# Optimization experiments

Hardware: AMD Instinct MI355X
Metric: run time of the kernel (lower is better)

Reference implementation:

```python
import jax, jax.numpy as jnp
import numpy as np

TAU = 2.0      # LIF membrane time constant
VTH = 1.0      # spike threshold
ALPHA = 2.0    # surrogate-gradient sharpness (atan surrogate)
EPS = 1e-5     # BatchNorm eps

@jax.custom_vjp
def spike(u):
    return (u > 0.0).astype(u.dtype)

def _spike_fwd(u):
    return spike(u), u

def _spike_bwd(u, g):
    sg = ALPHA / (2.0 * (1.0 + (jnp.pi / 2.0 * ALPHA * u) ** 2))
    return (g * sg,)

spike.defvjp(_spike_fwd, _spike_bwd)

def lif_time(x):
    # x: [B,T,C,H,W] -> spikes [B,T,C,H,W]; hard-reset LIF, v0 = 0
    xT = jnp.moveaxis(x, 1, 0)  # [T,B,C,H,W]
    def step(v, xt):
        v = v + (xt - v) / TAU
        s = spike(v - VTH)
        return v * (1.0 - s), s
    _, sT = jax.lax.scan(step, jnp.zeros_like(xT[0]), xT)
    return jnp.moveaxis(sT, 0, 1)

def conv2d(x, w, stride, pad):
    return jax.lax.conv_general_dilated(
        x, w, (stride, stride), [(pad, pad), (pad, pad)],
        dimension_numbers=('NCHW', 'OIHW', 'NCHW'))

def bn(x, gamma, beta, mean, var):
    # inference-style BatchNorm2d with running stats; x: [N,C,H,W]
    inv = gamma * jax.lax.rsqrt(var + EPS)
    return x * inv[None, :, None, None] + (beta - mean * inv)[None, :, None, None]

def setup_inputs() -> dict:
    key = jax.random.key(0)
    ks = jax.random.split(key, 16)
    B, T, Cin, Cout, H, W = 16, 8, 128, 256, 56, 56
    d = {}
    d['x_spike'] = (jax.random.uniform(ks[0], (B, T, Cin, H, W)) < 0.2).astype(jnp.float32)
    d['conv1_w'] = jax.random.normal(ks[1], (Cout, Cin, 3, 3), dtype=jnp.float32) * 0.05
    d['conv2_w'] = jax.random.normal(ks[2], (Cout, Cout, 3, 3), dtype=jnp.float32) * 0.05
    d['ds_w'] = jax.random.normal(ks[3], (Cout, Cin, 1, 1), dtype=jnp.float32) * 0.05
    for i, p in enumerate(['n1', 'n2', 'nd']):
        d[p + '_gamma'] = 1.0 + 0.1 * jax.random.normal(ks[4 + i], (Cout,), dtype=jnp.float32)
        d[p + '_beta'] = 0.1 * jax.random.normal(ks[7 + i], (Cout,), dtype=jnp.float32)
        d[p + '_mean'] = 0.01 * jax.random.normal(ks[10 + i], (Cout,), dtype=jnp.float32)
        d[p + '_var'] = jax.random.uniform(ks[13 + i], (Cout,), minval=0.5, maxval=1.5)
    return d

def reference(x_spike, conv1_w, conv2_w, ds_w,
              n1_gamma, n1_beta, n1_mean, n1_var,
              n2_gamma, n2_beta, n2_mean, n2_var,
              nd_gamma, nd_beta, nd_mean, nd_var):
    B, T, Cin, H, W = x_spike.shape
    x_flat = x_spike.reshape(B * T, Cin, H, W)
    # downsample shortcut (1x1 conv stride 2 + BN)
    identity = bn(conv2d(x_flat, ds_w, 2, 0), nd_gamma, nd_beta, nd_mean, nd_var)
    # NOTE: original module runs lif_shortcut on identity but DISCARDS the result
    # (pure state side-effect); it does not affect the output, so it is omitted.
    out = bn(conv2d(x_flat, conv1_w, 2, 1), n1_gamma, n1_beta, n1_mean, n1_var)
    Cout, Ho, Wo = out.shape[1], out.shape[2], out.shape[3]
    out = lif_time(out.reshape(B, T, Cout, Ho, Wo))
    out = bn(conv2d(out.reshape(B * T, Cout, Ho, Wo), conv2_w, 1, 1),
             n2_gamma, n2_beta, n2_mean, n2_var) + identity
    return lif_time(out.reshape(B, T, Cout, Ho, Wo))
```

## Files before the change

kernel.cpp:

```cpp
#include <hip/hip_runtime.h>
#include <hip/hip_bf16.h>

#define CIN  128
#define CO   256
#define HIN  56
#define WIN  56
#define OH   28
#define OWW  28
#define P    784
#define HWIN 3136
#define PERT 200704

typedef __attribute__((ext_vector_type(4))) float f32x4;
typedef __attribute__((ext_vector_type(4))) int   i32x4;

__device__ __forceinline__ i32x4 mfma_i8_64(i32x4 a, i32x4 b, i32x4 c) {
    return __builtin_amdgcn_mfma_i32_16x16x64_i8(a, b, c, 0, 0, 0);
}

__device__ __forceinline__ void gld_lds16(const void* g, void* l) {
    __builtin_amdgcn_global_load_lds(
        (const __attribute__((address_space(1))) void*)g,
        (__attribute__((address_space(3))) void*)l, 16, 0, 0);
}

__global__ __launch_bounds__(256) void k_prep_bias(
    const float* __restrict__ g1, const float* __restrict__ b1,
    const float* __restrict__ m1, const float* __restrict__ v1,
    const float* __restrict__ g2, const float* __restrict__ b2,
    const float* __restrict__ m2, const float* __restrict__ v2,
    const float* __restrict__ gd, const float* __restrict__ bd,
    const float* __restrict__ md, const float* __restrict__ vd,
    float* __restrict__ inv1o, float* __restrict__ bias1o,
    float* __restrict__ inv2o, float* __restrict__ invdo,
    float* __restrict__ bias2o)
{
    int co = threadIdx.x;
    float inv1 = g1[co] / sqrtf(v1[co] + 1e-5f);
    float inv2 = g2[co] / sqrtf(v2[co] + 1e-5f);
    float invd = gd[co] / sqrtf(vd[co] + 1e-5f);
    inv1o[co]  = inv1;
    bias1o[co] = fmaf(-m1[co], inv1, b1[co]);
    inv2o[co]  = inv2;
    invdo[co]  = invd;
    bias2o[co] = fmaf(-m2[co], inv2, b2[co]) + fmaf(-md[co], invd, bd[co]);
}

__global__ __launch_bounds__(256) void k_prep_w1s(
    const float* __restrict__ w1, const float* __restrict__ inv1,
    float* __restrict__ qscale, float* __restrict__ scale1)
{
    int wv = (blockIdx.x * 256 + threadIdx.x) >> 6;
    int lane = threadIdx.x & 63;
    int co = wv;
    float iv = inv1[co];
    float m = 0.f;
    for (int k = lane; k < 1152; k += 64)
        m = fmaxf(m, fabsf(w1[(size_t)co * 1152 + k] * iv));
#pragma unroll
    for (int off = 32; off > 0; off >>= 1)
        m = fmaxf(m, __shfl_xor(m, off));
    if (lane == 0) {
        int s = (int)floorf(log2f(8355000.0f / m));
        if (s > 44) s = 44;
        qscale[co] = ldexpf(1.0f, s);
        scale1[co] = ldexpf(1.0f, -s);
    }
}

__global__ __launch_bounds__(256) void k_prep_w1i8(
    const float* __restrict__ w1, const float* __restrict__ inv1,
    const float* __restrict__ qscale,
    signed char* __restrict__ pa, signed char* __restrict__ pb,
    signed char* __restrict__ pc)
{
    int i = blockIdx.x * 256 + threadIdx.x;
    if (i >= 18432) return;
    int tap = i >> 11;
    int r   = i & 2047;
    int kg  = r >> 10;
    int r2  = r & 1023;
    int lane = r2 & 63;
    int cf  = r2 >> 6;
    int co  = cf * 16 + (lane & 15);
    int ci0 = kg * 64 + (lane >> 4) * 16;
    float iv = inv1[co], q = qscale[co];
#pragma unroll
    for (int j = 0; j < 16; j++) {
        float w = w1[((size_t)co * CIN + ci0 + j) * 9 + tap] * iv;
        int W = __float2int_rn(w * q);
        int d0 = ((W & 0xFF) ^ 0x80) - 0x80;  W = (W - d0) / 256;
        int d1 = ((W & 0xFF) ^ 0x80) - 0x80;  W = (W - d1) / 256;
        size_t idx = (size_t)i * 16 + j;
        pa[idx] = (signed char)W;
        pb[idx] = (signed char)d1;
        pc[idx] = (signed char)d0;
    }
}

__global__ __launch_bounds__(256) void k_prep_w2s(
    const float* __restrict__ w2, const float* __restrict__ inv2,
    const float* __restrict__ wd, const float* __restrict__ invd,
    float* __restrict__ qscale, float* __restrict__ scale2)
{
    int wv = (blockIdx.x * 256 + threadIdx.x) >> 6;
    int lane = threadIdx.x & 63;
    int co = wv;
    float iv2 = inv2[co], ivd = invd[co];
    float m = 0.f;
    for (int k = lane; k < 2304; k += 64)
        m = fmaxf(m, fabsf(w2[(size_t)co * 2304 + k] * iv2));
    for (int k = lane; k < 128; k += 64)
        m = fmaxf(m, fabsf(wd[(size_t)co * 128 + k] * ivd));
#pragma unroll
    for (int off = 32; off > 0; off >>= 1)
        m = fmaxf(m, __shfl_xor(m, off));
    if (lane == 0) {
        int s = (int)floorf(log2f(8355000.0f / m));
        if (s > 40) s = 40;
        qscale[co] = ldexpf(1.0f, s);
        scale2[co] = ldexpf(1.0f, -s);
    }
}

__global__ __launch_bounds__(256) void k_prep_w2i8(
    const float* __restrict__ w2, const float* __restrict__ inv2,
    const float* __restrict__ qscale,
    signed char* __restrict__ pa, signed char* __restrict__ pb,
    signed char* __restrict__ pc)
{
    int i = blockIdx.x * 256 + threadIdx.x;
    if (i >= 36864) return;
    int tap = i >> 12;
    int r   = i & 4095;
    int kg  = r >> 10;
    int r2  = r & 1023;
    int cf  = r2 >> 6;
    int lane = r2 & 63;
    int co  = cf * 16 + (lane & 15);
    int ci0 = kg * 64 + (lane >> 4) * 16;
    float iv = inv2[co], q = qscale[co];
#pragma unroll
    for (int j = 0; j < 16; j++) {
        float w = w2[((size_t)co * CO + ci0 + j) * 9 + tap] * iv;
        int W = __float2int_rn(w * q);
        int d0 = ((W & 0xFF) ^ 0x80) - 0x80;  W = (W - d0) / 256;
        int d1 = ((W & 0xFF) ^ 0x80) - 0x80;  W = (W - d1) / 256;
        size_t idx = (size_t)i * 16 + j;
        pa[idx] = (signed char)W;
        pb[idx] = (signed char)d1;
        pc[idx] = (signed char)d0;
    }
}

__global__ __launch_bounds__(256) void k_prep_wdi8(
    const float* __restrict__ wd, const float* __restrict__ invd,
    const float* __restrict__ qscale,
    signed char* __restrict__ pa, signed char* __restrict__ pb,
    signed char* __restrict__ pc)
{
    int i = blockIdx.x * 256 + threadIdx.x;
    if (i >= 2048) return;
    int kg  = i >> 10;
    int r2  = i & 1023;
    int cf  = r2 >> 6;
    int lane = r2 & 63;
    int co  = cf * 16 + (lane & 15);
    int ci0 = kg * 64 + (lane >> 4) * 16;
    float iv = invd[co], q = qscale[co];
#pragma unroll
    for (int j = 0; j < 16; j++) {
        float w = wd[(size_t)co * CIN + ci0 + j] * iv;
        int W = __float2int_rn(w * q);
        int d0 = ((W & 0xFF) ^ 0x80) - 0x80;  W = (W - d0) / 256;
        int d1 = ((W & 0xFF) ^ 0x80) - 0x80;  W = (W - d1) / 256;
        size_t idx = (size_t)i * 16 + j;
        pa[idx] = (signed char)W;
        pb[idx] = (signed char)d1;
        pc[idx] = (signed char)d0;
    }
}

__global__ __launch_bounds__(256) void k_pack1(
    const float* __restrict__ x, unsigned int* __restrict__ xt_p)
{
    int i = blockIdx.x * 256 + threadIdx.x;
    int pos = i % HWIN;
    int nw  = i / HWIN;
    int w   = nw & 3;
    int n   = nw >> 2;
    const float* xp = x + ((size_t)n * CIN + w * 32) * HWIN + pos;
    unsigned int word = 0;
#pragma unroll
    for (int ci = 0; ci < 32; ci++)
        if (xp[(size_t)ci * HWIN] != 0.f) word |= (1u << ci);
    xt_p[((size_t)n * HWIN + pos) * 4 + w] = word;
}

__global__ __launch_bounds__(256) void k_conv1_mfma(
    const unsigned int* __restrict__ xt_p,
    const signed char* __restrict__ pa,
    const signed char* __restrict__ pb,
    const signed char* __restrict__ pc,
    const float* __restrict__ scale1,
    const float* __restrict__ bias1,
    float* __restrict__ out)
{
    __shared__ unsigned int XWP[2][522 * 2];

    const int n    = blockIdx.x / 7;
    const int rt   = blockIdx.x - n * 7;
    const int r0   = rt * 4;
    const int tid  = threadIdx.x;
    const int wave = tid >> 6;
    const int lane = tid & 63;
    const int l15  = lane & 15;
    const int quad = lane >> 4;
    const int cf   = blockIdx.y * 4 + wave;

    const unsigned int* xp_n = xt_p + (size_t)n * HWIN * 4;
    for (int i = tid; i < 513; i += 256) {
        int row = i / 57, c = i - row * 57;
        int irow = 2 * r0 - 1 + row;
        int iw   = c - 1;
        uint4 val = {0u, 0u, 0u, 0u};
        if (irow >= 0 && iw >= 0)
            val = *(const uint4*)(xp_n + (size_t)(irow * WIN + iw) * 4);
        int base = row * 58 + c;
        XWP[0][base * 2 + 0] = val.x;
        XWP[0][base * 2 + 1] = val.y;
        XWP[1][base * 2 + 0] = val.z;
        XWP[1][base * 2 + 1] = val.w;
    }
    __syncthreads();

    int ib[7];
#pragma unroll
    for (int f = 0; f < 7; f++) {
        int pos = f * 16 + l15;
        int rr = pos / 28, cc = pos - rr * 28;
        ib[f] = (2 * rr) * 58 + 2 * cc;
    }

    const int  qh = quad >> 1;
    const int  ql = (quad & 1) * 16;

    i32x4 accA[7], accB[7], accC[7];
#pragma unroll
    for (int f = 0; f < 7; f++) {
        accA[f] = (i32x4){0, 0, 0, 0};
        accB[f] = (i32x4){0, 0, 0, 0};
        accC[f] = (i32x4){0, 0, 0, 0};
    }

    i32x4 wa, wb, wc, na, nb, nc;
    {
        size_t b0 = (size_t)cf * 1024 + lane * 16;
        wa = *(const i32x4*)(pa + b0);
        wb = *(const i32x4*)(pb + b0);
        wc = *(const i32x4*)(pc + b0);
        na = wa; nb = wb; nc = wc;
    }

    for (int kg = 0; kg < 2; kg++) {
        for (int tap = 0; tap < 9; tap++) {
            int rd = kg * 9 + tap;
            if (rd < 17) {
                int rn = rd + 1, kn = rn / 9, tn = rn - kn * 9;
                size_t b0 = ((size_t)(tn * 2 + kn) * 16 + cf) * 1024 + lane * 16;
                na = *(const i32x4*)(pa + b0);
                nb = *(const i32x4*)(pb + b0);
                nc = *(const i32x4*)(pc + b0);
            }
            const int kh = tap / 3, kw = tap - kh * 3;
            const int tapoff = kh * 58 + kw;
#pragma unroll
            for (int f = 0; f < 7; f++) {
                int base = ib[f] + tapoff;
                uint2 pr = *(const uint2*)&XWP[kg][base * 2];
                unsigned int w32  = qh ? pr.y : pr.x;
                unsigned int bits = (w32 >> ql) & 0xFFFFu;
                uint4 u;
                u.x = ((bits & 15u)         * 0x00204081u) & 0x01010101u;
                u.y = (((bits >> 4) & 15u)  * 0x00204081u) & 0x01010101u;
                u.z = (((bits >> 8) & 15u)  * 0x00204081u) & 0x01010101u;
                u.w = ((bits >> 12)         * 0x00204081u) & 0x01010101u;
                union { uint4 q; i32x4 v; } cv;
                cv.q = u;
                accA[f] = mfma_i8_64(wa, cv.v, accA[f]);
                accB[f] = mfma_i8_64(wb, cv.v, accB[f]);
                accC[f] = mfma_i8_64(wc, cv.v, accC[f]);
            }
            wa = na; wb = nb; wc = nc;
        }
    }

#pragma unroll
    for (int f = 0; f < 7; f++) {
        int pg = rt * 112 + f * 16 + l15;
#pragma unroll
        for (int reg = 0; reg < 4; reg++) {
            int co = cf * 16 + quad * 4 + reg;
            float hi = (float)accA[f][reg];
            float mi = (float)accB[f][reg];
            float lo = (float)accC[f][reg];
            float val = fmaf(hi, 65536.f, fmaf(mi, 256.f, lo));
            out[((size_t)n * CO + co) * P + pg] = fmaf(val, scale1[co], bias1[co]);
        }
    }
}

__global__ __launch_bounds__(256) void k_lif1t(
    const float* __restrict__ pre, unsigned char* __restrict__ st)
{
    __shared__ unsigned short T[16 * 68];
    const int b   = blockIdx.x;
    const int co0 = blockIdx.y * 64;
    const int kg  = blockIdx.y;
    const int p0  = blockIdx.z * 16;
    const int tid  = threadIdx.x;
    const int pcol = tid & 15;
    const int g    = tid >> 4;
    const int pos = p0 + g;
    const int oh  = pos / 28, ow = pos - oh * 28;
    const int f8  = ((((oh + 1) * 30 + ow + 1) >> 1) & 3);
    const int no  = (pcol >> 2) ^ f8;
    const int wb  = (pcol & 3) * 4;
    float v[4] = {0.f, 0.f, 0.f, 0.f};
    for (int t = 0; t < 8; t++) {
        const float* src = pre + (((size_t)(b * 8 + t)) * CO + co0) * P + p0;
        unsigned short s[4];
#pragma unroll
        for (int j = 0; j < 4; j++) {
            int co = g + 16 * j;
            float xv = src[(size_t)co * P + pcol];
            v[j] = v[j] + (xv - v[j]) * 0.5f;
            bool sp = v[j] > 1.0f;
            s[j] = sp ? 1 : 0;
            if (sp) v[j] = 0.f;
        }
        __syncthreads();
#pragma unroll
        for (int j = 0; j < 4; j++) T[pcol * 68 + g + 16 * j] = s[j];
        __syncthreads();
        unsigned char* dst = st + (((size_t)(b * 8 + t) * 4 + kg) * P + pos) * 64
                               + no * 16 + wb;
        uchar4 ov;
        ov.x = (unsigned char)T[g * 68 + pcol * 4 + 0];
        ov.y = (unsigned char)T[g * 68 + pcol * 4 + 1];
        ov.z = (unsigned char)T[g * 68 + pcol * 4 + 2];
        ov.w = (unsigned char)T[g * 68 + pcol * 4 + 3];
        *(uchar4*)dst = ov;
    }
}

__global__ __launch_bounds__(256) void k_conv2_mfma(
    const unsigned char* __restrict__ spike_t,
    const unsigned int* __restrict__ xt_p,
    const signed char* __restrict__ p2a,
    const signed char* __restrict__ p2b,
    const signed char* __restrict__ p2c,
    const signed char* __restrict__ pda,
    const signed char* __restrict__ pdb,
    const signed char* __restrict__ pdc,
    const float* __restrict__ scale2,
    const float* __restrict__ bias2,
    float* __restrict__ out)
{
    __shared__ unsigned char SB[2 * 11520];
    __shared__ unsigned int  XW2[4 * 112];

    const int n    = blockIdx.x / 7;
    const int rt   = blockIdx.x - n * 7;
    const int r0   = rt * 4;
    const int tid  = threadIdx.x;
    const int wave = tid >> 6;
    const int lane = tid & 63;
    const int l15  = lane & 15;
    const int quad = lane >> 4;
    const int cf0  = blockIdx.y * 8 + wave * 2;

    {
        uint4 z = {0u, 0u, 0u, 0u};
        for (int i = tid; i < 1440; i += 256) ((uint4*)SB)[i] = z;
    }
    for (int i = tid; i < 112; i += 256) {
        int r = i / 28, c = i - r * 28;
        uint4 w4 = *(const uint4*)(xt_p + ((size_t)n * HWIN
                    + (2 * (r0 + r)) * WIN + 2 * c) * 4);
        XW2[0 * 112 + i] = w4.x;
        XW2[1 * 112 + i] = w4.y;
        XW2[2 * 112 + i] = w4.z;
        XW2[3 * 112 + i] = w4.w;
    }
    __syncthreads();

    int  g_irow[3], g_lds[3];
    bool g_ok[3];
    int  g_half[3];
#pragma unroll
    for (int k = 0; k < 3; k++) {
        int idx  = wave * 3 + k;
        int row  = idx >> 1, half = idx & 1;
        int irow = r0 - 1 + row;
        g_irow[k] = irow;
        g_half[k] = half;
        g_ok[k]   = ((unsigned)irow < 28u) && (half == 0 || lane < 48);
        g_lds[k]  = row * 1920 + 64 + half * 1024;
    }
    const char* sp_n = (const char*)spike_t + (size_t)n * 4 * P * 64;

#pragma unroll
    for (int k = 0; k < 3; k++)
        if (g_ok[k])
            gld_lds16(sp_n + (size_t)g_irow[k] * 1792 + g_half[k] * 1024 + lane * 16,
                      (char*)SB + g_lds[k]);

    int ib[7];
#pragma unroll
    for (int f = 0; f < 7; f++) {
        int pos = f * 16 + l15;
        int rr = pos / 28, cc = pos - rr * 28;
        ib[f] = rr * 30 + cc;
    }

    i32x4 acc[3][2][7];
#pragma unroll
    for (int p = 0; p < 3; p++)
#pragma unroll
        for (int g = 0; g < 2; g++)
#pragma unroll
            for (int f = 0; f < 7; f++) acc[p][g][f] = (i32x4){0, 0, 0, 0};

    for (int kg = 0; kg < 2; kg++) {
        size_t b0 = ((size_t)kg * 16 + cf0) * 1024 + (size_t)lane * 16;
        i32x4 d0[2], d1[2], d2[2];
#pragma unroll
        for (int g = 0; g < 2; g++) {
            d0[g] = *(const i32x4*)(pda + b0 + (size_t)g * 1024);
            d1[g] = *(const i32x4*)(pdb + b0 + (size_t)g * 1024);
            d2[g] = *(const i32x4*)(pdc + b0 + (size_t)g * 1024);
        }
        const int wsel = (kg * 2 + (quad >> 1)) * 112;
        const int shv  = (quad & 1) * 16;
#pragma unroll
        for (int f = 0; f < 7; f++) {
            unsigned int w32  = XW2[wsel + f * 16 + l15];
            unsigned int bits = (w32 >> shv) & 0xFFFFu;
            uint4 u;
            u.x = ((bits & 15u)         * 0x00204081u) & 0x01010101u;
            u.y = (((bits >> 4) & 15u)  * 0x00204081u) & 0x01010101u;
            u.z = (((bits >> 8) & 15u)  * 0x00204081u) & 0x01010101u;
            u.w = ((bits >> 12)         * 0x00204081u) & 0x01010101u;
            union { uint4 q; i32x4 v; } cv;
            cv.q = u;
#pragma unroll
            for (int g = 0; g < 2; g++) {
                acc[0][g][f] = mfma_i8_64(d0[g], cv.v, acc[0][g][f]);
                acc[1][g][f] = mfma_i8_64(d1[g], cv.v, acc[1][g][f]);
                acc[2][g][f] = mfma_i8_64(d2[g], cv.v, acc[2][g][f]);
            }
        }
    }
    __syncthreads();

    i32x4 cw[2][3], nx[2][3];
#pragma unroll
    for (int g = 0; g < 2; g++) {
        size_t b0 = ((size_t)(cf0 + g)) * 1024 + (size_t)lane * 16;
        cw[g][0] = *(const i32x4*)(p2a + b0);
        cw[g][1] = *(const i32x4*)(p2b + b0);
        cw[g][2] = *(const i32x4*)(p2c + b0);
        nx[g][0] = cw[g][0]; nx[g][1] = cw[g][1]; nx[g][2] = cw[g][2];
    }

    for (int c = 0; c < 4; c++) {
        if (c < 3) {
            const char* base = sp_n + (size_t)(c + 1) * 50176;
            char* dstb = (char*)SB + ((c + 1) & 1) * 11520;
#pragma unroll
            for (int k = 0; k < 3; k++)
                if (g_ok[k])
                    gld_lds16(base + (size_t)g_irow[k] * 1792 + g_half[k] * 1024 + lane * 16,
                              dstb + g_lds[k]);
        }
        const int bufsh = (c & 1) * 11520;
        for (int tap = 0; tap < 9; tap++) {
            int rd = c * 9 + tap;
            if (rd < 35) {
                int rn = rd + 1, cn = rn / 9, tn = rn - cn * 9;
                size_t b0 = ((size_t)(tn * 4 + cn) * 16 + cf0) * 1024
                          + (size_t)lane * 16;
#pragma unroll
                for (int g = 0; g < 2; g++) {
                    nx[g][0] = *(const i32x4*)(p2a + b0 + (size_t)g * 1024);
                    nx[g][1] = *(const i32x4*)(p2b + b0 + (size_t)g * 1024);
                    nx[g][2] = *(const i32x4*)(p2c + b0 + (size_t)g * 1024);
                }
            }
            const int kh = tap / 3, kw = tap - kh * 3;
            const int tapoff = kh * 30 + kw;
#pragma unroll
            for (int f = 0; f < 7; f++) {
                int slot = ib[f] + tapoff;
                int sw   = (slot >> 1) & 3;
                i32x4 bfr = *(const i32x4*)(
                    SB + bufsh + slot * 64 + ((quad ^ sw) * 16));
#pragma unroll
                for (int g = 0; g < 2; g++) {
                    acc[0][g][f] = mfma_i8_64(cw[g][0], bfr, acc[0][g][f]);
                    acc[1][g][f] = mfma_i8_64(cw[g][1], bfr, acc[1][g][f]);
                    acc[2][g][f] = mfma_i8_64(cw[g][2], bfr, acc[2][g][f]);
                }
            }
#pragma unroll
            for (int g = 0; g < 2; g++) {
                cw[g][0] = nx[g][0]; cw[g][1] = nx[g][1]; cw[g][2] = nx[g][2];
            }
        }
        __syncthreads();
    }

#pragma unroll
    for (int g = 0; g < 2; g++)
#pragma unroll
        for (int f = 0; f < 7; f++) {
            int pg = rt * 112 + f * 16 + l15;
#pragma unroll
            for (int reg = 0; reg < 4; reg++) {
                int co = (cf0 + g) * 16 + quad * 4 + reg;
                float A  = (float)acc[0][g][f][reg];
                float Bv = (float)acc[1][g][f][reg];
                float Cv = (float)acc[2][g][f][reg];
                float val = fmaf(A, 65536.f, fmaf(Bv, 256.f, Cv));
                out[((size_t)n * CO + co) * P + pg] = fmaf(val, scale2[co], bias2[co]);
            }
        }
}

__global__ __launch_bounds__(256) void k_lif4(const float4* __restrict__ in,
                                              float4* __restrict__ out)
{
    const int q = PERT / 4;
    const int i = blockIdx.x * 256 + threadIdx.x;
    const int b = i / q;
    const int r = i - b * q;
    const float4* pi = in  + (size_t)(b * 8) * q + r;
    float4*       po = out + (size_t)(b * 8) * q + r;
    float v0 = 0.f, v1 = 0.f, v2 = 0.f, v3 = 0.f;
#pragma unroll
    for (int t = 0; t < 8; t++) {
        float4 xt = pi[(size_t)t * q];
        float4 s;
        v0 = v0 + (xt.x - v0) * 0.5f; s.x = (v0 > 1.0f) ? 1.f : 0.f; if (v0 > 1.0f) v0 = 0.f;
        v1 = v1 + (xt.y - v1) * 0.5f; s.y = (v1 > 1.0f) ? 1.f : 0.f; if (v1 > 1.0f) v1 = 0.f;
        v2 = v2 + (xt.z - v2) * 0.5f; s.z = (v2 > 1.0f) ? 1.f : 0.f; if (v2 > 1.0f) v2 = 0.f;
        v3 = v3 + (xt.w - v3) * 0.5f; s.w = (v3 > 1.0f) ? 1.f : 0.f; if (v3 > 1.0f) v3 = 0.f;
        po[(size_t)t * q] = s;
    }
}

extern "C" void kernel_launch(void* const* d_in, const int* in_sizes, int n_in,
                              void* d_out, int out_size, void* d_ws, size_t ws_size,
                              hipStream_t stream) {
    const float* x   = (const float*)d_in[0];
    const float* w1  = (const float*)d_in[1];
    const float* w2  = (const float*)d_in[2];
    const float* wd  = (const float*)d_in[3];
    const float* n1g = (const float*)d_in[4];
    const float* n1b = (const float*)d_in[5];
    const float* n1m = (const float*)d_in[6];
    const float* n1v = (const float*)d_in[7];
    const float* n2g = (const float*)d_in[8];
    const float* n2b = (const float*)d_in[9];
    const float* n2m = (const float*)d_in[10];
    const float* n2v = (const float*)d_in[11];
    const float* ndg = (const float*)d_in[12];
    const float* ndb = (const float*)d_in[13];
    const float* ndm = (const float*)d_in[14];
    const float* ndv = (const float*)d_in[15];

    float* out = (float*)d_out;

    char* w = (char*)d_ws;
    unsigned char*  spike_t = (unsigned char*)w;
    signed char*    p2a     = (signed char*)(w + 25690112);
    signed char*    p2b     = (signed char*)(w + 26279936);
    signed char*    p2c     = (signed char*)(w + 26869760);
    signed char*    pa      = (signed char*)(w + 27459584);
    signed char*    pb      = (signed char*)(w + 27754496);
    signed char*    pc      = (signed char*)(w + 28049408);
    signed char*    pda     = (signed char*)(w + 28344320);
    signed char*    pdb     = (signed char*)(w + 28377088);
    signed char*    pdc     = (signed char*)(w + 28409856);
    float*          qscale1 = (float*)(w + 28442624);
    float*          scale1f = (float*)(w + 28443648);
    float*          qscale2 = (float*)(w + 28444672);
    float*          scale2f = (float*)(w + 28445696);
    float*          bias2   = (float*)(w + 28446720);
    float*          bias1   = (float*)(w + 28447744);
    float*          inv1    = (float*)(w + 28448768);
    float*          inv2    = (float*)(w + 28449792);
    float*          invd    = (float*)(w + 28450816);
    unsigned int*   xt_p    = (unsigned int*)(w + 28451840);

    k_prep_bias<<<1, 256, 0, stream>>>(n1g, n1b, n1m, n1v,
                                       n2g, n2b, n2m, n2v,
                                       ndg, ndb, ndm, ndv,
                                       inv1, bias1, inv2, invd, bias2);
    k_prep_w1s<<<64, 256, 0, stream>>>(w1, inv1, qscale1, scale1f);
    k_prep_w1i8<<<72, 256, 0, stream>>>(w1, inv1, qscale1, pa, pb, pc);
    k_prep_w2s<<<64, 256, 0, stream>>>(w2, inv2, wd, invd, qscale2, scale2f);
    k_prep_w2i8<<<144, 256, 0, stream>>>(w2, inv2, qscale2, p2a, p2b, p2c);
    k_prep_wdi8<<<8, 256, 0, stream>>>(wd, invd, qscale2, pda, pdb, pdc);

    k_pack1<<<(128 * 4 * HWIN) / 256, 256, 0, stream>>>(x, xt_p);
    k_conv1_mfma<<<dim3(896, 4), 256, 0, stream>>>(
        xt_p, pa, pb, pc, scale1f, bias1, out);
    k_lif1t<<<dim3(16, 4, 49), 256, 0, stream>>>(out, spike_t);
    k_conv2_mfma<<<dim3(896, 2), 256, 0, stream>>>(
        spike_t, xt_p, p2a, p2b, p2c, pda, pdb, pdc, scale2f, bias2, out);
    k_lif4<<<(16 * (PERT / 4)) / 256, 256, 0, stream>>>(
        (const float4*)out, (float4*)out);
}
```

Baseline: 726.1 us.

## Merge prep kernels, stage all conv2 channel groups in LDS, add MFMA priority

Seven small weight-prep and packing kernels are merged into two launches, with the BN inverse recomputed inline instead of stored, which cuts launch overhead. Conv2 now loads all four input-channel groups into a quadrupled LDS buffer up front and runs one flat 36-step loop with no per-chunk barriers. Downsample weights are hoisted into registers before the loop. s_setprio is raised around MFMA groups in both convs. The larger LDS footprint (about 46KB) may lower occupancy, and the extra registers for hoisted weights may raise register pressure.

```diff
diff --git a/kernel.cpp b/kernel.cpp
--- a/kernel.cpp
+++ b/kernel.cpp
@@ -1,12 +1,9 @@
 #include <hip/hip_runtime.h>
-#include <hip/hip_bf16.h>
 
 #define CIN  128
 #define CO   256
 #define HIN  56
 #define WIN  56
-#define OH   28
-#define OWW  28
 #define P    784
 #define HWIN 3136
 #define PERT 200704
@@ -24,177 +21,163 @@
         (__attribute__((address_space(3))) void*)l, 16, 0, 0);
 }
 
-__global__ __launch_bounds__(256) void k_prep_bias(
+__global__ __launch_bounds__(256) void k_prepA(
     const float* __restrict__ g1, const float* __restrict__ b1,
     const float* __restrict__ m1, const float* __restrict__ v1,
     const float* __restrict__ g2, const float* __restrict__ b2,
     const float* __restrict__ m2, const float* __restrict__ v2,
     const float* __restrict__ gd, const float* __restrict__ bd,
     const float* __restrict__ md, const float* __restrict__ vd,
-    float* __restrict__ inv1o, float* __restrict__ bias1o,
-    float* __restrict__ inv2o, float* __restrict__ invdo,
-    float* __restrict__ bias2o)
+    const float* __restrict__ w1, const float* __restrict__ w2,
+    const float* __restrict__ wd,
+    float* __restrict__ bias1, float* __restrict__ bias2,
+    float* __restrict__ qscale1, float* __restrict__ scale1,
+    float* __restrict__ qscale2, float* __restrict__ scale2)
 {
-    int co = threadIdx.x;
-    float inv1 = g1[co] / sqrtf(v1[co] + 1e-5f);
-    float inv2 = g2[co] / sqrtf(v2[co] + 1e-5f);
-    float invd = gd[co] / sqrtf(vd[co] + 1e-5f);
-    inv1o[co]  = inv1;
-    bias1o[co] = fmaf(-m1[co], inv1, b1[co]);
-    inv2o[co]  = inv2;
-    invdo[co]  = invd;
-    bias2o[co] = fmaf(-m2[co], inv2, b2[co]) + fmaf(-md[co], invd, bd[co]);
-}
-
-__global__ __launch_bounds__(256) void k_prep_w1s(
-    const float* __restrict__ w1, const float* __restrict__ inv1,
-    float* __restrict__ qscale, float* __restrict__ scale1)
-{
-    int wv = (blockIdx.x * 256 + threadIdx.x) >> 6;
-    int lane = threadIdx.x & 63;
-    int co = wv;
-    float iv = inv1[co];
-    float m = 0.f;
-    for (int k = lane; k < 1152; k += 64)
-        m = fmaxf(m, fabsf(w1[(size_t)co * 1152 + k] * iv));
-#pragma unroll
-    for (int off = 32; off > 0; off >>= 1)
-        m = fmaxf(m, __shfl_xor(m, off));
-    if (lane == 0) {
-        int s = (int)floorf(log2f(8355000.0f / m));
-        if (s > 44) s = 44;
-        qscale[co] = ldexpf(1.0f, s);
-        scale1[co] = ldexpf(1.0f, -s);
-    }
-}
-
-__global__ __launch_bounds__(256) void k_prep_w1i8(
-    const float* __restrict__ w1, const float* __restrict__ inv1,
-    const float* __restrict__ qscale,
+    const int bid = blockIdx.x;
+    if (bid == 0) {
+        int co = threadIdx.x;
+        float inv1 = g1[co] / sqrtf(v1[co] + 1e-5f);
+        float inv2 = g2[co] / sqrtf(v2[co] + 1e-5f);
+        float invd = gd[co] / sqrtf(vd[co] + 1e-5f);
+        bias1[co] = fmaf(-m1[co], inv1, b1[co]);
+        bias2[co] = fmaf(-m2[co], inv2, b2[co]) + fmaf(-md[co], invd, bd[co]);
+        return;
+    }
+    const int lane = threadIdx.x & 63;
+    if (bid <= 64) {
+        int co = (bid - 1) * 4 + (threadIdx.x >> 6);
+        float iv = g1[co] / sqrtf(v1[co] + 1e-5f);
+        float m = 0.f;
+        for (int k = lane; k < 1152; k += 64)
+            m = fmaxf(m, fabsf(w1[(size_t)co * 1152 + k] * iv));
+#pragma unroll
+        for (int off = 32; off > 0; off >>= 1)
+            m = fmaxf(m, __shfl_xor(m, off));
+        if (lane == 0) {
+            int s = (int)floorf(log2f(8355000.0f / m));
+            if (s > 44) s = 44;
+            qscale1[co] = ldexpf(1.0f, s);
+            scale1[co]  = ldexpf(1.0f, -s);
+        }
+    } else {
+        int co = (bid - 65) * 4 + (threadIdx.x >> 6);
+        float iv2 = g2[co] / sqrtf(v2[co] + 1e-5f);
+        float ivd = gd[co] / sqrtf(vd[co] + 1e-5f);
+        float m = 0.f;
+        for (int k = lane; k < 2304; k += 64)
+            m = fmaxf(m, fabsf(w2[(size_t)co * 2304 + k] * iv2));
+        for (int k = lane; k < 128; k += 64)
+            m = fmaxf(m, fabsf(wd[(size_t)co * 128 + k] * ivd));
+#pragma unroll
+        for (int off = 32; off > 0; off >>= 1)
+            m = fmaxf(m, __shfl_xor(m, off));
+        if (lane == 0) {
+            int s = (int)floorf(log2f(8355000.0f / m));
+            if (s > 40) s = 40;
+            qscale2[co] = ldexpf(1.0f, s);
+            scale2[co]  = ldexpf(1.0f, -s);
+        }
+    }
+}
+
+__global__ __launch_bounds__(256) void k_prepB(
+    const float* __restrict__ w1, const float* __restrict__ w2,
+    const float* __restrict__ wd,
+    const float* __restrict__ n1g, const float* __restrict__ n1v,
+    const float* __restrict__ n2g, const float* __restrict__ n2v,
+    const float* __restrict__ ndg, const float* __restrict__ ndv,
+    const float* __restrict__ qscale1, const float* __restrict__ qscale2,
     signed char* __restrict__ pa, signed char* __restrict__ pb,
-    signed char* __restrict__ pc)
-{
-    int i = blockIdx.x * 256 + threadIdx.x;
-    if (i >= 18432) return;
-    int tap = i >> 11;
-    int r   = i & 2047;
-    int kg  = r >> 10;
-    int r2  = r & 1023;
-    int lane = r2 & 63;
-    int cf  = r2 >> 6;
-    int co  = cf * 16 + (lane & 15);
-    int ci0 = kg * 64 + (lane >> 4) * 16;
-    float iv = inv1[co], q = qscale[co];
-#pragma unroll
-    for (int j = 0; j < 16; j++) {
-        float w = w1[((size_t)co * CIN + ci0 + j) * 9 + tap] * iv;
-        int W = __float2int_rn(w * q);
-        int d0 = ((W & 0xFF) ^ 0x80) - 0x80;  W = (W - d0) / 256;
-        int d1 = ((W & 0xFF) ^ 0x80) - 0x80;  W = (W - d1) / 256;
-        size_t idx = (size_t)i * 16 + j;
-        pa[idx] = (signed char)W;
-        pb[idx] = (signed char)d1;
-        pc[idx] = (signed char)d0;
-    }
-}
-
-__global__ __launch_bounds__(256) void k_prep_w2s(
-    const float* __restrict__ w2, const float* __restrict__ inv2,
-    const float* __restrict__ wd, const float* __restrict__ invd,
-    float* __restrict__ qscale, float* __restrict__ scale2)
-{
-    int wv = (blockIdx.x * 256 + threadIdx.x) >> 6;
-    int lane = threadIdx.x & 63;
-    int co = wv;
-    float iv2 = inv2[co], ivd = invd[co];
-    float m = 0.f;
-    for (int k = lane; k < 2304; k += 64)
-        m = fmaxf(m, fabsf(w2[(size_t)co * 2304 + k] * iv2));
-    for (int k = lane; k < 128; k += 64)
-        m = fmaxf(m, fabsf(wd[(size_t)co * 128 + k] * ivd));
-#pragma unroll
-    for (int off = 32; off > 0; off >>= 1)
-        m = fmaxf(m, __shfl_xor(m, off));
-    if (lane == 0) {
-        int s = (int)floorf(log2f(8355000.0f / m));
-        if (s > 40) s = 40;
-        qscale[co] = ldexpf(1.0f, s);
-        scale2[co] = ldexpf(1.0f, -s);
-    }
-}
-
-__global__ __launch_bounds__(256) void k_prep_w2i8(
-    const float* __restrict__ w2, const float* __restrict__ inv2,
-    const float* __restrict__ qscale,
-    signed char* __restrict__ pa, signed char* __restrict__ pb,
-    signed char* __restrict__ pc)
-{
-    int i = blockIdx.x * 256 + threadIdx.x;
-    if (i >= 36864) return;
-    int tap = i >> 12;
-    int r   = i & 4095;
-    int kg  = r >> 10;
-    int r2  = r & 1023;
-    int cf  = r2 >> 6;
-    int lane = r2 & 63;
-    int co  = cf * 16 + (lane & 15);
-    int ci0 = kg * 64 + (lane >> 4) * 16;
-    float iv = inv2[co], q = qscale[co];
-#pragma unroll
-    for (int j = 0; j < 16; j++) {
-        float w = w2[((size_t)co * CO + ci0 + j) * 9 + tap] * iv;
-        int W = __float2int_rn(w * q);
-        int d0 = ((W & 0xFF) ^ 0x80) - 0x80;  W = (W - d0) / 256;
-        int d1 = ((W & 0xFF) ^ 0x80) - 0x80;  W = (W - d1) / 256;
-        size_t idx = (size_t)i * 16 + j;
-        pa[idx] = (signed char)W;
-        pb[idx] = (signed char)d1;
-        pc[idx] = (signed char)d0;
-    }
-}
-
-__global__ __launch_bounds__(256) void k_prep_wdi8(
-    const float* __restrict__ wd, const float* __restrict__ invd,
-    const float* __restrict__ qscale,
-    signed char* __restrict__ pa, signed char* __restrict__ pb,
-    signed char* __restrict__ pc)
-{
-    int i = blockIdx.x * 256 + threadIdx.x;
-    if (i >= 2048) return;
-    int kg  = i >> 10;
-    int r2  = i & 1023;
-    int cf  = r2 >> 6;
-    int lane = r2 & 63;
-    int co  = cf * 16 + (lane & 15);
-    int ci0 = kg * 64 + (lane >> 4) * 16;
-    float iv = invd[co], q = qscale[co];
-#pragma unroll
-    for (int j = 0; j < 16; j++) {
-        float w = wd[(size_t)co * CIN + ci0 + j] * iv;
-        int W = __float2int_rn(w * q);
-        int d0 = ((W & 0xFF) ^ 0x80) - 0x80;  W = (W - d0) / 256;
-        int d1 = ((W & 0xFF) ^ 0x80) - 0x80;  W = (W - d1) / 256;
-        size_t idx = (size_t)i * 16 + j;
-        pa[idx] = (signed char)W;
-        pb[idx] = (signed char)d1;
-        pc[idx] = (signed char)d0;
-    }
-}
-
-__global__ __launch_bounds__(256) void k_pack1(
+    signed char* __restrict__ pc,
+    signed char* __restrict__ p2a, signed char* __restrict__ p2b,
+    signed char* __restrict__ p2c,
+    signed char* __restrict__ pda, signed char* __restrict__ pdb,
+    signed char* __restrict__ pdc,
     const float* __restrict__ x, unsigned int* __restrict__ xt_p)
 {
-    int i = blockIdx.x * 256 + threadIdx.x;
-    int pos = i % HWIN;
-    int nw  = i / HWIN;
-    int w   = nw & 3;
-    int n   = nw >> 2;
-    const float* xp = x + ((size_t)n * CIN + w * 32) * HWIN + pos;
-    unsigned int word = 0;
-#pragma unroll
-    for (int ci = 0; ci < 32; ci++)
-        if (xp[(size_t)ci * HWIN] != 0.f) word |= (1u << ci);
-    xt_p[((size_t)n * HWIN + pos) * 4 + w] = word;
+    const int bid = blockIdx.x;
+    if (bid < 72) {
+        int i = bid * 256 + threadIdx.x;
+        if (i >= 18432) return;
+        int tap = i >> 11;
+        int r   = i & 2047;
+        int kg  = r >> 10;
+        int r2  = r & 1023;
+        int cf  = r2 >> 6;
+        int lane = r2 & 63;
+        int co  = cf * 16 + (lane & 15);
+        int ci0 = kg * 64 + (lane >> 4) * 16;
+        float iv = n1g[co] / sqrtf(n1v[co] + 1e-5f);
+        float q  = qscale1[co];
+#pragma unroll
+        for (int j = 0; j < 16; j++) {
+            float w = w1[((size_t)co * CIN + ci0 + j) * 9 + tap] * iv;
+            int W = __float2int_rn(w * q);
+            int d0 = ((W & 0xFF) ^ 0x80) - 0x80;  W = (W - d0) / 256;
+            int d1 = ((W & 0xFF) ^ 0x80) - 0x80;  W = (W - d1) / 256;
+            size_t idx = (size_t)i * 16 + j;
+            pa[idx] = (signed char)W;
+            pb[idx] = (signed char)d1;
+            pc[idx] = (signed char)d0;
+        }
+    } else if (bid < 216) {
+        int i = (bid - 72) * 256 + threadIdx.x;
+        int tap = i >> 12;
+        int r   = i & 4095;
+        int kg  = r >> 10;
+        int r2  = r & 1023;
+        int cf  = r2 >> 6;
+        int lane = r2 & 63;
+        int co  = cf * 16 + (lane & 15);
+        int ci0 = kg * 64 + (lane >> 4) * 16;
+        float iv = n2g[co] / sqrtf(n2v[co] + 1e-5f);
+        float q  = qscale2[co];
+#pragma unroll
+        for (int j = 0; j < 16; j++) {
+            float w = w2[((size_t)co * CO + ci0 + j) * 9 + tap] * iv;
+            int W = __float2int_rn(w * q);
+            int d0 = ((W & 0xFF) ^ 0x80) - 0x80;  W = (W - d0) / 256;
+            int d1 = ((W & 0xFF) ^ 0x80) - 0x80;  W = (W - d1) / 256;
+            size_t idx = (size_t)i * 16 + j;
+            p2a[idx] = (signed char)W;
+            p2b[idx] = (signed char)d1;
+            p2c[idx] = (signed char)d0;
+        }
+    } else if (bid < 224) {
+        int i = (bid - 216) * 256 + threadIdx.x;
+        int kg  = i >> 10;
+        int r2  = i & 1023;
+        int cf  = r2 >> 6;
+        int lane = r2 & 63;
+        int co  = cf * 16 + (lane & 15);
+        int ci0 = kg * 64 + (lane >> 4) * 16;
+        float iv = ndg[co] / sqrtf(ndv[co] + 1e-5f);
+        float q  = qscale2[co];
+#pragma unroll
+        for (int j = 0; j < 16; j++) {
+            float w = wd[(size_t)co * CIN + ci0 + j] * iv;
+            int W = __float2int_rn(w * q);
+            int d0 = ((W & 0xFF) ^ 0x80) - 0x80;  W = (W - d0) / 256;
+            int d1 = ((W & 0xFF) ^ 0x80) - 0x80;  W = (W - d1) / 256;
+            size_t idx = (size_t)i * 16 + j;
+            pda[idx] = (signed char)W;
+            pdb[idx] = (signed char)d1;
+            pdc[idx] = (signed char)d0;
+        }
+    } else {
+        int i = (bid - 224) * 256 + threadIdx.x;
+        int pos = i % HWIN;
+        int nw  = i / HWIN;
+        int w   = nw & 3;
+        int n   = nw >> 2;
+        const float* xp = x + ((size_t)n * CIN + w * 32) * HWIN + pos;
+        unsigned int word = 0;
+#pragma unroll
+        for (int ci = 0; ci < 32; ci++)
+            if (xp[(size_t)ci * HWIN] != 0.f) word |= (1u << ci);
+        xt_p[((size_t)n * HWIN + pos) * 4 + w] = word;
+    }
 }
 
 __global__ __launch_bounds__(256) void k_conv1_mfma(
@@ -287,9 +270,11 @@
                 u.w = ((bits >> 12)         * 0x00204081u) & 0x01010101u;
                 union { uint4 q; i32x4 v; } cv;
                 cv.q = u;
+                __builtin_amdgcn_s_setprio(1);
                 accA[f] = mfma_i8_64(wa, cv.v, accA[f]);
                 accB[f] = mfma_i8_64(wb, cv.v, accB[f]);
                 accC[f] = mfma_i8_64(wc, cv.v, accC[f]);
+                __builtin_amdgcn_s_setprio(0);
             }
             wa = na; wb = nb; wc = nc;
         }
@@ -367,7 +352,7 @@
     const float* __restrict__ bias2,
     float* __restrict__ out)
 {
-    __shared__ unsigned char SB[2 * 11520];
+    __shared__ unsigned char SB[4 * 11520];
     __shared__ unsigned int  XW2[4 * 112];
 
     const int n    = blockIdx.x / 7;
@@ -382,7 +367,7 @@
 
     {
         uint4 z = {0u, 0u, 0u, 0u};
-        for (int i = tid; i < 1440; i += 256) ((uint4*)SB)[i] = z;
+        for (int i = tid; i < 2880; i += 256) ((uint4*)SB)[i] = z;
     }
     for (int i = tid; i < 112; i += 256) {
         int r = i / 28, c = i - r * 28;
@@ -395,26 +380,34 @@
     }
     __syncthreads();
 
-    int  g_irow[3], g_lds[3];
-    bool g_ok[3];
-    int  g_half[3];
+    i32x4 dw[2][3][2];
+#pragma unroll
+    for (int kg = 0; kg < 2; kg++) {
+        size_t b0 = ((size_t)kg * 16 + cf0) * 1024 + (size_t)lane * 16;
+#pragma unroll
+        for (int g = 0; g < 2; g++) {
+            dw[kg][0][g] = *(const i32x4*)(pda + b0 + (size_t)g * 1024);
+            dw[kg][1][g] = *(const i32x4*)(pdb + b0 + (size_t)g * 1024);
+            dw[kg][2][g] = *(const i32x4*)(pdc + b0 + (size_t)g * 1024);
+        }
+    }
+
+    const char* sp_n = (const char*)spike_t + (size_t)n * 4 * P * 64;
 #pragma unroll
     for (int k = 0; k < 3; k++) {
         int idx  = wave * 3 + k;
         int row  = idx >> 1, half = idx & 1;
         int irow = r0 - 1 + row;
-        g_irow[k] = irow;
-        g_half[k] = half;
-        g_ok[k]   = ((unsigned)irow < 28u) && (half == 0 || lane < 48);
-        g_lds[k]  = row * 1920 + 64 + half * 1024;
-    }
-    const char* sp_n = (const char*)spike_t + (size_t)n * 4 * P * 64;
-
-#pragma unroll
-    for (int k = 0; k < 3; k++)
-        if (g_ok[k])
-            gld_lds16(sp_n + (size_t)g_irow[k] * 1792 + g_half[k] * 1024 + lane * 16,
-                      (char*)SB + g_lds[k]);
+        bool ok  = ((unsigned)irow < 28u) && (half == 0 || lane < 48);
+        int ldso = row * 1920 + 64 + half * 1024;
+        if (ok) {
+#pragma unroll
+            for (int kg = 0; kg < 4; kg++)
+                gld_lds16(sp_n + (size_t)kg * 50176 + (size_t)irow * 1792
+                              + half * 1024 + lane * 16,
+                          (char*)SB + kg * 11520 + ldso);
+        }
+    }
 
     int ib[7];
 #pragma unroll
@@ -432,15 +425,8 @@
 #pragma unroll
             for (int f = 0; f < 7; f++) acc[p][g][f] = (i32x4){0, 0, 0, 0};
 
+#pragma unroll
     for (int kg = 0; kg < 2; kg++) {
-        size_t b0 = ((size_t)kg * 16 + cf0) * 1024 + (size_t)lane * 16;
-        i32x4 d0[2], d1[2], d2[2];
-#pragma unroll
-        for (int g = 0; g < 2; g++) {
-            d0[g] = *(const i32x4*)(pda + b0 + (size_t)g * 1024);
-            d1[g] = *(const i32x4*)(pdb + b0 + (size_t)g * 1024);
-            d2[g] = *(const i32x4*)(pdc + b0 + (size_t)g * 1024);
-        }
         const int wsel = (kg * 2 + (quad >> 1)) * 112;
         const int shv  = (quad & 1) * 16;
 #pragma unroll
@@ -454,12 +440,14 @@
             u.w = ((bits >> 12)         * 0x00204081u) & 0x01010101u;
             union { uint4 q; i32x4 v; } cv;
             cv.q = u;
+            __builtin_amdgcn_s_setprio(1);
 #pragma unroll
             for (int g = 0; g < 2; g++) {
-                acc[0][g][f] = mfma_i8_64(d0[g], cv.v, acc[0][g][f]);
-                acc[1][g][f] = mfma_i8_64(d1[g], cv.v, acc[1][g][f]);
-                acc[2][g][f] = mfma_i8_64(d2[g], cv.v, acc[2][g][f]);
+                acc[0][g][f] = mfma_i8_64(dw[kg][0][g], cv.v, acc[0][g][f]);
+                acc[1][g][f] = mfma_i8_64(dw[kg][1][g], cv.v, acc[1][g][f]);
+                acc[2][g][f] = mfma_i8_64(dw[kg][2][g], cv.v, acc[2][g][f]);
             }
+            __builtin_amdgcn_s_setprio(0);
         }
     }
     __syncthreads();
@@ -474,51 +462,40 @@
         nx[g][0] = cw[g][0]; nx[g][1] = cw[g][1]; nx[g][2] = cw[g][2];
     }
 
-    for (int c = 0; c < 4; c++) {
-        if (c < 3) {
-            const char* base = sp_n + (size_t)(c + 1) * 50176;
-            char* dstb = (char*)SB + ((c + 1) & 1) * 11520;
-#pragma unroll
-            for (int k = 0; k < 3; k++)
-                if (g_ok[k])
-                    gld_lds16(base + (size_t)g_irow[k] * 1792 + g_half[k] * 1024 + lane * 16,
-                              dstb + g_lds[k]);
-        }
-        const int bufsh = (c & 1) * 11520;
-        for (int tap = 0; tap < 9; tap++) {
-            int rd = c * 9 + tap;
-            if (rd < 35) {
-                int rn = rd + 1, cn = rn / 9, tn = rn - cn * 9;
-                size_t b0 = ((size_t)(tn * 4 + cn) * 16 + cf0) * 1024
-                          + (size_t)lane * 16;
-#pragma unroll
-                for (int g = 0; g < 2; g++) {
-                    nx[g][0] = *(const i32x4*)(p2a + b0 + (size_t)g * 1024);
-                    nx[g][1] = *(const i32x4*)(p2b + b0 + (size_t)g * 1024);
-                    nx[g][2] = *(const i32x4*)(p2c + b0 + (size_t)g * 1024);
-                }
+    for (int rd = 0; rd < 36; rd++) {
+        if (rd < 35) {
+            size_t b0 = ((size_t)(rd + 1) * 16 + cf0) * 1024
+                      + (size_t)lane * 16;
+#pragma unroll
+            for (int g = 0; g < 2; g++) {
+                nx[g][0] = *(const i32x4*)(p2a + b0 + (size_t)g * 1024);
+                nx[g][1] = *(const i32x4*)(p2b + b0 + (size_t)g * 1024);
+                nx[g][2] = *(const i32x4*)(p2c + b0 + (size_t)g * 1024);
             }
-            const int kh = tap / 3, kw = tap - kh * 3;
-            const int tapoff = kh * 30 + kw;
-#pragma unroll
-            for (int f = 0; f < 7; f++) {
-                int slot = ib[f] + tapoff;
-                int sw   = (slot >> 1) & 3;
-                i32x4 bfr = *(const i32x4*)(
-                    SB + bufsh + slot * 64 + ((quad ^ sw) * 16));
-#pragma unroll
-                for (int g = 0; g < 2; g++) {
-                    acc[0][g][f] = mfma_i8_64(cw[g][0], bfr, acc[0][g][f]);
-                    acc[1][g][f] = mfma_i8_64(cw[g][1], bfr, acc[1][g][f]);
-                    acc[2][g][f] = mfma_i8_64(cw[g][2], bfr, acc[2][g][f]);
-                }
+        }
+        const int tap = rd >> 2, kg = rd & 3;
+        const int kh = tap / 3, kw = tap - kh * 3;
+        const int tapoff = kh * 30 + kw;
+        const int sbase  = kg * 11520;
+#pragma unroll
+        for (int f = 0; f < 7; f++) {
+            int slot = ib[f] + tapoff;
+            int sw   = (slot >> 1) & 3;
+            i32x4 bfr = *(const i32x4*)(
+                SB + sbase + slot * 64 + ((quad ^ sw) * 16));
+            __builtin_amdgcn_s_setprio(1);
+#pragma unroll
+            for (int g = 0; g < 2; g++) {
+                acc[0][g][f] = mfma_i8_64(cw[g][0], bfr, acc[0][g][f]);
+                acc[1][g][f] = mfma_i8_64(cw[g][1], bfr, acc[1][g][f]);
+                acc[2][g][f] = mfma_i8_64(cw[g][2], bfr, acc[2][g][f]);
             }
-#pragma unroll
-            for (int g = 0; g < 2; g++) {
-                cw[g][0] = nx[g][0]; cw[g][1] = nx[g][1]; cw[g][2] = nx[g][2];
-            }
-        }
-        __syncthreads();
+            __builtin_amdgcn_s_setprio(0);
+        }
+#pragma unroll
+        for (int g = 0; g < 2; g++) {
+            cw[g][0] = nx[g][0]; cw[g][1] = nx[g][1]; cw[g][2] = nx[g][2];
+        }
     }
 
 #pragma unroll
@@ -599,22 +576,15 @@
     float*          scale2f = (float*)(w + 28445696);
     float*          bias2   = (float*)(w + 28446720);
     float*          bias1   = (float*)(w + 28447744);
-    float*          inv1    = (float*)(w + 28448768);
-    float*          inv2    = (float*)(w + 28449792);
-    float*          invd    = (float*)(w + 28450816);
     unsigned int*   xt_p    = (unsigned int*)(w + 28451840);
 
-    k_prep_bias<<<1, 256, 0, stream>>>(n1g, n1b, n1m, n1v,
-                                       n2g, n2b, n2m, n2v,
-                                       ndg, ndb, ndm, ndv,
-                                       inv1, bias1, inv2, invd, bias2);
-    k_prep_w1s<<<64, 256, 0, stream>>>(w1, inv1, qscale1, scale1f);
-    k_prep_w1i8<<<72, 256, 0, stream>>>(w1, inv1, qscale1, pa, pb, pc);
-    k_prep_w2s<<<64, 256, 0, stream>>>(w2, inv2, wd, invd, qscale2, scale2f);
-    k_prep_w2i8<<<144, 256, 0, stream>>>(w2, inv2, qscale2, p2a, p2b, p2c);
-    k_prep_wdi8<<<8, 256, 0, stream>>>(wd, invd, qscale2, pda, pdb, pdc);
-
-    k_pack1<<<(128 * 4 * HWIN) / 256, 256, 0, stream>>>(x, xt_p);
+    k_prepA<<<129, 256, 0, stream>>>(
+        n1g, n1b, n1m, n1v, n2g, n2b, n2m, n2v, ndg, ndb, ndm, ndv,
+        w1, w2, wd, bias1, bias2, qscale1, scale1f, qscale2, scale2f);
+    k_prepB<<<224 + (128 * 4 * HWIN) / 256, 256, 0, stream>>>(
+        w1, w2, wd, n1g, n1v, n2g, n2v, ndg, ndv, qscale1, qscale2,
+        pa, pb, pc, p2a, p2b, p2c, pda, pdb, pdc, x, xt_p);
+
     k_conv1_mfma<<<dim3(896, 4), 256, 0, stream>>>(
         xt_p, pa, pb, pc, scale1f, bias1, out);
     k_lif1t<<<dim3(16, 4, 49), 256, 0, stream>>>(out, spike_t);
```

Measured after the change: 710.3 us. 2.2% less time.
